# Optimization experiments

Measured on AMD Instinct MI355X. Metric: run time of the kernel, lower is better.

Reference implementation:

```python
import jax, jax.numpy as jnp
import numpy as np

B, C, H, W = 8, 64, 256, 256
M1, M2 = 16, 16


def setup_inputs() -> dict:
    key = jax.random.key(0)
    k1, k2, k3 = jax.random.split(key, 3)
    scale = 1.0 / (C * C)
    x = jax.random.normal(k1, (B, C, H, W), dtype=jnp.float32)
    # torch.rand(..., dtype=cfloat) -> uniform [0,1) real and imag parts
    w_real = scale * jax.random.uniform(k2, (C, C, M1, M2), dtype=jnp.float32)
    w_imag = scale * jax.random.uniform(k3, (C, C, M1, M2), dtype=jnp.float32)
    return {"x": x, "w_real": w_real, "w_imag": w_imag}


def reference(x, w_real, w_imag):
    m1, m2 = w_real.shape[2], w_real.shape[3]
    h, w = x.shape[-2], x.shape[-1]
    weights = w_real + 1j * w_imag  # (Cin, Cout, m1, m2) complex64
    # rfftn over axes (-1,-2): real->complex transform on the LAST listed axis (-2),
    # so x_ft has shape (B, C, H//2+1, W) — matching torch exactly.
    x_ft = jnp.fft.rfftn(x, axes=(-1, -2))
    out_low = jnp.einsum('bixy,ioxy->boxy', x_ft[..., :m1, :m2], weights)
    out_ft = jnp.zeros_like(x_ft).at[..., :m1, :m2].set(out_low)
    # irfftn with s=(H,W) over default axes (-2,-1): irfft on the last axis
    # truncates it to W//2+1 — same quirky-but-valid behavior as the torch code.
    return jnp.fft.irfftn(out_ft, s=(h, w))
```

## Files before the change

kernel.cpp:

```cpp
#include <hip/hip_runtime.h>
#include <math.h>

#define NIMG 512
#define HW   65536

__global__ __launch_bounds__(256)
void twinit(float* __restrict__ tw_g) {
    int idx = blockIdx.x * 256 + threadIdx.x;
    int n = idx >> 4, k = idx & 15;
    float s, c;
    sincospif(((k * n) & 255) * (1.0f / 128.0f), &s, &c);
    tw_g[idx * 2]     = c;
    tw_g[idx * 2 + 1] = s;
}

__global__ __launch_bounds__(256, 4)
void stageA(const float* __restrict__ x, const float* __restrict__ tw_g,
            float* __restrict__ xf_re, float* __restrict__ xf_im) {
    __shared__ __attribute__((aligned(16))) float tw[2048];
    __shared__ __attribute__((aligned(16))) float cbuf[8192];
    const int tid = threadIdx.x;
    const int img = blockIdx.x;

    ((float4*)tw)[tid]       = ((const float4*)tw_g)[tid];
    ((float4*)tw)[tid + 256] = ((const float4*)tw_g)[tid + 256];
    __syncthreads();

    const float* xp = x + (size_t)img * HW + tid;
    float cr[16], ci[16];
    #pragma unroll
    for (int u = 0; u < 16; ++u) { cr[u] = 0.0f; ci[u] = 0.0f; }

    const float4* tw4 = (const float4*)tw;
    #pragma unroll 2
    for (int hb = 0; hb < 64; ++hb) {
        float a = xp[hb * 256];
        float b = xp[(hb + 64) * 256];
        float c = xp[(hb + 128) * 256];
        float d = xp[(hb + 192) * 256];
        float p = a + c, m = a - c, q = b + d, r = b - d;
        float s0 = p + q, s2 = p - q;
        #pragma unroll
        for (int qq = 0; qq < 8; ++qq) {
            float4 e = tw4[hb * 8 + qq];
            float se = (qq & 1) ? s2 : s0;
            float si = (qq & 1) ? r : -r;
            cr[2*qq]     += se * e.x;
            ci[2*qq]     -= se * e.y;
            cr[2*qq + 1] += m  * e.z + si * e.w;
            ci[2*qq + 1] += si * e.z - m  * e.w;
        }
    }

    float2* cb = (float2*)cbuf;
    #pragma unroll
    for (int u = 0; u < 16; ++u)
        cb[u * 256 + tid] = make_float2(cr[u], ci[u]);
    __syncthreads();

    const int u = tid >> 4, v = tid & 15;
    const bool odd = (v & 1) != 0;
    const float t = (v & 2) ? -1.0f : 1.0f;
    const float2* twc = (const float2*)tw;
    float xr = 0.0f, xi = 0.0f;
    #pragma unroll 2
    for (int wb = 0; wb < 64; ++wb) {
        float2 Ca = cb[u * 256 + wb];
        float2 Cb = cb[u * 256 + wb + 64];
        float2 Cc = cb[u * 256 + wb + 128];
        float2 Cd = cb[u * 256 + wb + 192];
        float pr = Ca.x + Cc.x, pi_ = Ca.y + Cc.y;
        float mr = Ca.x - Cc.x, mi  = Ca.y - Cc.y;
        float qr = Cb.x + Cd.x, qi  = Cb.y + Cd.y;
        float rr = Cb.x - Cd.x, ri  = Cb.y - Cd.y;
        float X1 = odd ? mr : pr;
        float X2 = odd ? ri : qr;
        float Y1 = odd ? mi : pi_;
        float Y2 = odd ? -rr : qi;
        float sr = X1 + t * X2;
        float si = Y1 + t * Y2;
        float2 e = twc[wb * 16 + v];
        xr += sr * e.x + si * e.y;
        xi += si * e.x - sr * e.y;
    }
    xf_re[img * 256 + tid] = xr;
    xf_im[img * 256 + tid] = xi;
}

__global__ __launch_bounds__(256)
void stageB(const float* __restrict__ wr, const float* __restrict__ wi,
            const float* __restrict__ xf_re, const float* __restrict__ xf_im,
            float* __restrict__ s_re, float* __restrict__ s_im) {
    const int tid = threadIdx.x;
    const int o = blockIdx.x >> 3;
    const int b = blockIdx.x & 7;
    float sr = 0.0f, si = 0.0f;
    #pragma unroll 4
    for (int i = 0; i < 64; ++i) {
        float wre = wr[((i * 64 + o) << 8) + tid];
        float wim = wi[((i * 64 + o) << 8) + tid];
        float xr  = xf_re[((b * 64 + i) << 8) + tid];
        float xi  = xf_im[((b * 64 + i) << 8) + tid];
        sr += xr * wre - xi * wim;
        si += xr * wim + xi * wre;
    }
    s_re[((b * 64 + o) << 8) + tid] = sr;
    s_im[((b * 64 + o) << 8) + tid] = si;
}

__global__ __launch_bounds__(256, 4)
void stageC(const float* __restrict__ s_re, const float* __restrict__ s_im,
            const float* __restrict__ tw_g, float* __restrict__ out) {
    __shared__ __attribute__((aligned(16))) float tw[2048];
    __shared__ __attribute__((aligned(16))) float sl[512];
    const int tid = threadIdx.x;
    const int img = blockIdx.x;

    ((float4*)tw)[tid]       = ((const float4*)tw_g)[tid];
    ((float4*)tw)[tid + 256] = ((const float4*)tw_g)[tid + 256];
    {
        int v = tid & 15;
        float scale = (v == 0 ? 1.0f : 2.0f) * (1.0f / 65536.0f);
        sl[tid * 2]     = s_re[img * 256 + tid] * scale;
        sl[tid * 2 + 1] = s_im[img * 256 + tid] * scale;
    }
    __syncthreads();

    float tr[16], ti[16];
    #pragma unroll
    for (int u = 0; u < 16; ++u) { tr[u] = 0.0f; ti[u] = 0.0f; }

    float bs, bc;
    sincospif(tid * (1.0f / 128.0f), &bs, &bc);
    float ec = 1.0f, es = 0.0f;
    for (int v = 0; v < 16; ++v) {
        #pragma unroll
        for (int u = 0; u < 16; ++u) {
            float a = sl[(u * 16 + v) * 2];
            float b = sl[(u * 16 + v) * 2 + 1];
            tr[u] += a * ec - b * es;
            ti[u] += a * es + b * ec;
        }
        float nc = ec * bc - es * bs;
        float ns = ec * bs + es * bc;
        ec = nc; es = ns;
    }

    float* op = out + (size_t)img * HW + tid;
    const float4* tw4 = (const float4*)tw;
    #pragma unroll 2
    for (int hb = 0; hb < 64; ++hb) {
        float o0 = 0.f, o1 = 0.f, o2 = 0.f, o3 = 0.f;
        #pragma unroll
        for (int qq = 0; qq < 8; ++qq) {
            float4 e = tw4[hb * 8 + qq];
            float pre = tr[2*qq]   * e.x - ti[2*qq]   * e.y;
            float pro = tr[2*qq+1] * e.z - ti[2*qq+1] * e.w;
            float pio = tr[2*qq+1] * e.w + ti[2*qq+1] * e.z;
            o0 += pre + pro;
            o2 += pre - pro;
            float g1 = pre - pio, g3 = pre + pio;
            if (qq & 1) { o1 -= g1; o3 -= g3; }
            else        { o1 += g1; o3 += g3; }
        }
        op[hb * 256]         = o0;
        op[(hb + 64) * 256]  = o1;
        op[(hb + 128) * 256] = o2;
        op[(hb + 192) * 256] = o3;
    }
}

extern "C" void kernel_launch(void* const* d_in, const int* in_sizes, int n_in,
                              void* d_out, int out_size, void* d_ws, size_t ws_size,
                              hipStream_t stream) {
    const float* x  = (const float*)d_in[0];
    const float* wr = (const float*)d_in[1];
    const float* wi = (const float*)d_in[2];
    float* out = (float*)d_out;
    float* ws  = (float*)d_ws;

    float* xf_re = ws;
    float* xf_im = ws + 131072;
    float* s_re  = ws + 262144;
    float* s_im  = ws + 393216;
    float* tw_g  = ws + 524288;

    twinit<<<4, 256, 0, stream>>>(tw_g);
    stageA<<<NIMG, 256, 0, stream>>>(x, tw_g, xf_re, xf_im);
    stageB<<<NIMG, 256, 0, stream>>>(wr, wi, xf_re, xf_im, s_re, s_im);
    stageC<<<NIMG, 256, 0, stream>>>(s_re, s_im, tw_g, out);
}
```

Before: 283.1 us.

## Fuse mode mixing with inverse transform and compute twiddles in-kernel

Merges the channel-mixing stage into the inverse-transform kernel, so each block computes its own spectral coefficients and writes the output image directly. This removes the intermediate spectrum round trip and one launch. The separate twiddle-init kernel is dropped and each block now computes its twiddle table in shared memory with sincospif. StageA batches four rows of loads per iteration for more memory-level parallelism, launch bounds drop to 2 waves per SIMD, and block-to-(batch, channel) mapping is swizzled for better weight reuse in cache. The trade-off is redundant twiddle computation per block and possibly lower occupancy.

```diff
diff --git a/kernel.cpp b/kernel.cpp
--- a/kernel.cpp
+++ b/kernel.cpp
@@ -4,26 +4,23 @@
 #define NIMG 512
 #define HW   65536
 
-__global__ __launch_bounds__(256)
-void twinit(float* __restrict__ tw_g) {
-    int idx = blockIdx.x * 256 + threadIdx.x;
-    int n = idx >> 4, k = idx & 15;
-    float s, c;
-    sincospif(((k * n) & 255) * (1.0f / 128.0f), &s, &c);
-    tw_g[idx * 2]     = c;
-    tw_g[idx * 2 + 1] = s;
-}
-
-__global__ __launch_bounds__(256, 4)
-void stageA(const float* __restrict__ x, const float* __restrict__ tw_g,
+__global__ __launch_bounds__(256, 2)
+void stageA(const float* __restrict__ x,
             float* __restrict__ xf_re, float* __restrict__ xf_im) {
     __shared__ __attribute__((aligned(16))) float tw[2048];
     __shared__ __attribute__((aligned(16))) float cbuf[8192];
     const int tid = threadIdx.x;
     const int img = blockIdx.x;
 
-    ((float4*)tw)[tid]       = ((const float4*)tw_g)[tid];
-    ((float4*)tw)[tid + 256] = ((const float4*)tw_g)[tid + 256];
+    #pragma unroll
+    for (int j = 0; j < 4; ++j) {
+        int idx = (tid << 2) | j;
+        int n = idx >> 4, k = idx & 15;
+        float s, c;
+        sincospif(((k * n) & 255) * (1.0f / 128.0f), &s, &c);
+        tw[idx * 2]     = c;
+        tw[idx * 2 + 1] = s;
+    }
     __syncthreads();
 
     const float* xp = x + (size_t)img * HW + tid;
@@ -32,23 +29,31 @@
     for (int u = 0; u < 16; ++u) { cr[u] = 0.0f; ci[u] = 0.0f; }
 
     const float4* tw4 = (const float4*)tw;
-    #pragma unroll 2
-    for (int hb = 0; hb < 64; ++hb) {
-        float a = xp[hb * 256];
-        float b = xp[(hb + 64) * 256];
-        float c = xp[(hb + 128) * 256];
-        float d = xp[(hb + 192) * 256];
-        float p = a + c, m = a - c, q = b + d, r = b - d;
-        float s0 = p + q, s2 = p - q;
+    #pragma unroll 1
+    for (int hb = 0; hb < 64; hb += 4) {
+        float av[4], bv[4], cv[4], dv[4];
         #pragma unroll
-        for (int qq = 0; qq < 8; ++qq) {
-            float4 e = tw4[hb * 8 + qq];
-            float se = (qq & 1) ? s2 : s0;
-            float si = (qq & 1) ? r : -r;
-            cr[2*qq]     += se * e.x;
-            ci[2*qq]     -= se * e.y;
-            cr[2*qq + 1] += m  * e.z + si * e.w;
-            ci[2*qq + 1] += si * e.z - m  * e.w;
+        for (int j = 0; j < 4; ++j) {
+            av[j] = xp[(hb + j) * 256];
+            bv[j] = xp[(hb + j + 64) * 256];
+            cv[j] = xp[(hb + j + 128) * 256];
+            dv[j] = xp[(hb + j + 192) * 256];
+        }
+        #pragma unroll
+        for (int j = 0; j < 4; ++j) {
+            float p = av[j] + cv[j], m = av[j] - cv[j];
+            float q = bv[j] + dv[j], r = bv[j] - dv[j];
+            float s0 = p + q, s2 = p - q;
+            #pragma unroll
+            for (int qq = 0; qq < 8; ++qq) {
+                float4 e = tw4[(hb + j) * 8 + qq];
+                float se = (qq & 1) ? s2 : s0;
+                float si = (qq & 1) ? r : -r;
+                cr[2*qq]     += se * e.x;
+                ci[2*qq]     -= se * e.y;
+                cr[2*qq + 1] += m  * e.z + si * e.w;
+                ci[2*qq + 1] += si * e.z - m  * e.w;
+            }
         }
     }
 
@@ -77,25 +82,40 @@
         float X2 = odd ? ri : qr;
         float Y1 = odd ? mi : pi_;
         float Y2 = odd ? -rr : qi;
-        float sr = X1 + t * X2;
-        float si = Y1 + t * Y2;
+        float sr_ = X1 + t * X2;
+        float si_ = Y1 + t * Y2;
         float2 e = twc[wb * 16 + v];
-        xr += sr * e.x + si * e.y;
-        xi += si * e.x - sr * e.y;
+        xr += sr_ * e.x + si_ * e.y;
+        xi += si_ * e.x - sr_ * e.y;
     }
     xf_re[img * 256 + tid] = xr;
     xf_im[img * 256 + tid] = xi;
 }
 
-__global__ __launch_bounds__(256)
-void stageB(const float* __restrict__ wr, const float* __restrict__ wi,
-            const float* __restrict__ xf_re, const float* __restrict__ xf_im,
-            float* __restrict__ s_re, float* __restrict__ s_im) {
+__global__ __launch_bounds__(256, 2)
+void stageBC(const float* __restrict__ wr, const float* __restrict__ wi,
+             const float* __restrict__ xf_re, const float* __restrict__ xf_im,
+             float* __restrict__ out) {
+    __shared__ __attribute__((aligned(16))) float tw[2048];
+    __shared__ __attribute__((aligned(16))) float sl[512];
     const int tid = threadIdx.x;
-    const int o = blockIdx.x >> 3;
-    const int b = blockIdx.x & 7;
+
+    #pragma unroll
+    for (int j = 0; j < 4; ++j) {
+        int idx = (tid << 2) | j;
+        int n = idx >> 4, k = idx & 15;
+        float s, c;
+        sincospif(((k * n) & 255) * (1.0f / 128.0f), &s, &c);
+        tw[idx * 2]     = c;
+        tw[idx * 2 + 1] = s;
+    }
+
+    const int g = blockIdx.x;
+    const int o = ((g & 7) << 3) | ((g >> 6) & 7);
+    const int b = (g >> 3) & 7;
+
     float sr = 0.0f, si = 0.0f;
-    #pragma unroll 4
+    #pragma unroll 8
     for (int i = 0; i < 64; ++i) {
         float wre = wr[((i * 64 + o) << 8) + tid];
         float wim = wi[((i * 64 + o) << 8) + tid];
@@ -104,25 +124,12 @@
         sr += xr * wre - xi * wim;
         si += xr * wim + xi * wre;
     }
-    s_re[((b * 64 + o) << 8) + tid] = sr;
-    s_im[((b * 64 + o) << 8) + tid] = si;
-}
 
-__global__ __launch_bounds__(256, 4)
-void stageC(const float* __restrict__ s_re, const float* __restrict__ s_im,
-            const float* __restrict__ tw_g, float* __restrict__ out) {
-    __shared__ __attribute__((aligned(16))) float tw[2048];
-    __shared__ __attribute__((aligned(16))) float sl[512];
-    const int tid = threadIdx.x;
-    const int img = blockIdx.x;
-
-    ((float4*)tw)[tid]       = ((const float4*)tw_g)[tid];
-    ((float4*)tw)[tid + 256] = ((const float4*)tw_g)[tid + 256];
     {
         int v = tid & 15;
         float scale = (v == 0 ? 1.0f : 2.0f) * (1.0f / 65536.0f);
-        sl[tid * 2]     = s_re[img * 256 + tid] * scale;
-        sl[tid * 2 + 1] = s_im[img * 256 + tid] * scale;
+        sl[tid * 2]     = sr * scale;
+        sl[tid * 2 + 1] = si * scale;
     }
     __syncthreads();
 
@@ -136,17 +143,17 @@
     for (int v = 0; v < 16; ++v) {
         #pragma unroll
         for (int u = 0; u < 16; ++u) {
-            float a = sl[(u * 16 + v) * 2];
-            float b = sl[(u * 16 + v) * 2 + 1];
-            tr[u] += a * ec - b * es;
-            ti[u] += a * es + b * ec;
+            float a  = sl[(u * 16 + v) * 2];
+            float b2 = sl[(u * 16 + v) * 2 + 1];
+            tr[u] += a * ec - b2 * es;
+            ti[u] += a * es + b2 * ec;
         }
         float nc = ec * bc - es * bs;
         float ns = ec * bs + es * bc;
         ec = nc; es = ns;
     }
 
-    float* op = out + (size_t)img * HW + tid;
+    float* op = out + (size_t)(b * 64 + o) * HW + tid;
     const float4* tw4 = (const float4*)tw;
     #pragma unroll 2
     for (int hb = 0; hb < 64; ++hb) {
@@ -181,12 +188,7 @@
 
     float* xf_re = ws;
     float* xf_im = ws + 131072;
-    float* s_re  = ws + 262144;
-    float* s_im  = ws + 393216;
-    float* tw_g  = ws + 524288;
 
-    twinit<<<4, 256, 0, stream>>>(tw_g);
-    stageA<<<NIMG, 256, 0, stream>>>(x, tw_g, xf_re, xf_im);
-    stageB<<<NIMG, 256, 0, stream>>>(wr, wi, xf_re, xf_im, s_re, s_im);
-    stageC<<<NIMG, 256, 0, stream>>>(s_re, s_im, tw_g, out);
+    stageA<<<NIMG, 256, 0, stream>>>(x, xf_re, xf_im);
+    stageBC<<<NIMG, 256, 0, stream>>>(wr, wi, xf_re, xf_im, out);
 }
```

After: 274.6 us. 3.0% less time.
